# Kernel optimization log

Measured on AMD Instinct MI355X. Metric: run time of the kernel, lower is better.

The kernel has to match this reference:

```python
import jax, jax.numpy as jnp
import numpy as np

H, D = 8, 8          # num_heads, hidden_size (head dim)
SCALE = 0.25         # Hopfield beta/scaling
STEPS = 3            # update_steps_max
LN_EPS = 1e-5


def ln(x, g, b):
    m = x.mean(-1, keepdims=True)
    v = ((x - m) ** 2).mean(-1, keepdims=True)
    return (x - m) * jax.lax.rsqrt(v + LN_EPS) * g + b


def setup_inputs() -> dict:
    key = jax.random.key(0)
    ks = jax.random.split(key, 8)
    B, N, E = 32, 512, 512
    P = H * D  # 64 virtual hopfield dim
    s = lambda k, shape: jax.random.normal(k, shape, jnp.float32) * 0.05
    return dict(
        x=jax.random.normal(ks[0], (B, N, E), jnp.float32),
        g_q=jnp.ones((E,), jnp.float32), b_q=jnp.zeros((E,), jnp.float32),
        g_k=jnp.ones((E,), jnp.float32), b_k=jnp.zeros((E,), jnp.float32),
        g_v=jnp.ones((E,), jnp.float32), b_v=jnp.zeros((E,), jnp.float32),
        Wq=s(ks[1], (P, E)), bq=jnp.zeros((P,), jnp.float32),
        Wk=s(ks[2], (P, E)), bk=jnp.zeros((P,), jnp.float32),
        Wv=s(ks[3], (P, E)), bv=jnp.zeros((P,), jnp.float32),
        Wo=s(ks[4], (E, P)), bo=jnp.zeros((E,), jnp.float32),
        Wl=s(ks[5], (1, N * E)), bl=jnp.zeros((1,), jnp.float32),
    )


def reference(x, g_q, b_q, g_k, b_k, g_v, b_v,
              Wq, bq, Wk, bk, Wv, bv, Wo, bo, Wl, bl):
    B, N, E = x.shape
    # LayerNorm on state (query), stored (key), projection (value) patterns
    q = (ln(x, g_q, b_q) @ Wq.T + bq).reshape(B, N, H, D)
    k = (ln(x, g_k, b_k) @ Wk.T + bk).reshape(B, N, H, D)
    v = (ln(x, g_v, b_v) @ Wv.T + bv).reshape(B, N, H, D)
    # iterative Hopfield retrieval: xi <- softmax(beta * xi K^T) K
    xi = q
    for _ in range(STEPS):
        a = jax.nn.softmax(SCALE * jnp.einsum('bihd,bjhd->bhij', xi, k), axis=-1)
        xi = jnp.einsum('bhij,bjhd->bihd', a, k)
    # final association with value patterns
    a = jax.nn.softmax(SCALE * jnp.einsum('bihd,bjhd->bhij', xi, k), axis=-1)
    o = jnp.einsum('bhij,bjhd->bihd', a, v).reshape(B, N, H * D)
    o = o @ Wo.T + bo              # (B, N, E) out projection
    y = o.reshape(B, N * E) @ Wl.T + bl  # (B, 1) classifier head
    return y.reshape(-1)           # flatten(start_dim=0) -> (B,)
```

## Files before the change

### kernel.cpp

```cpp
#include <hip/hip_runtime.h>

#define E_DIM 512
#define N_DIM 512
#define B_DIM 32
#define H_DIM 8
#define D_DIM 8
#define P3    192

typedef _Float16 half_t;
typedef __attribute__((ext_vector_type(2))) _Float16 half2v;
typedef __attribute__((ext_vector_type(4))) _Float16 half4v;
typedef __attribute__((ext_vector_type(8))) _Float16 half8v;
typedef __attribute__((ext_vector_type(4))) float f32x4;

#define XS_STRIDE 520

#define SM_KT0 0
#define SM_KB0 4800
#define SM_Z0  8896
#define SM_XI0 9408
#define SM_TOT 9936
#define KT_STRIDE 532

__device__ inline float block_reduce_256(float v) {
    __shared__ float red[4];
    #pragma unroll
    for (int m = 32; m >= 1; m >>= 1) v += __shfl_xor(v, m);
    int w = threadIdx.x >> 6;
    if ((threadIdx.x & 63) == 0) red[w] = v;
    __syncthreads();
    if (threadIdx.x == 0) v = red[0] + red[1] + red[2] + red[3];
    return v;
}

__device__ inline half8v cvt8(float4 a, float4 b) {
    half8v h;
    h[0] = (half_t)a.x; h[1] = (half_t)a.y; h[2] = (half_t)a.z; h[3] = (half_t)a.w;
    h[4] = (half_t)b.x; h[5] = (half_t)b.y; h[6] = (half_t)b.z; h[7] = (half_t)b.w;
    return h;
}

__device__ inline half2v pk2(float a, float b) {
    return __builtin_bit_cast(half2v, __builtin_amdgcn_cvt_pkrtz(a, b));
}

__global__ __launch_bounds__(256) void prep_w(const float* __restrict__ Wq,
                        const float* __restrict__ Wk, const float* __restrict__ Wv,
                        const float* __restrict__ gq, const float* __restrict__ gk,
                        const float* __restrict__ gv,
                        const float* __restrict__ bnq, const float* __restrict__ bnk,
                        const float* __restrict__ bnv,
                        const float* __restrict__ bq, const float* __restrict__ bk,
                        const float* __restrict__ bv,
                        const float* __restrict__ bl,
                        half_t* __restrict__ WthF, float* __restrict__ colsum,
                        float* __restrict__ b2, float* __restrict__ y,
                        float* __restrict__ c0acc) {
    int pp = blockIdx.x;
    int which = pp >> 6, p = pp & 63;
    int ct = pp >> 4, c16 = pp & 15;
    const float* W  = (which == 0) ? Wq  : (which == 1) ? Wk  : Wv;
    const float* g  = (which == 0) ? gq  : (which == 1) ? gk  : gv;
    const float* bn = (which == 0) ? bnq : (which == 1) ? bnk : bnv;
    const float* bb = (which == 0) ? bq  : (which == 1) ? bk  : bv;
    int t = threadIdx.x;
    if (pp == 0) {
        if (t < 32) y[t] = bl[0];
        if (t == 32) c0acc[0] = 0.f;
    }
    float cs = 0.f, dt = 0.f;
    #pragma unroll
    for (int l = 0; l < 2; ++l) {
        int e = t + l * 256;
        float wv = W[p * E_DIM + e];
        half_t wh = (half_t)(wv * g[e]);
        int k32 = e >> 5, g2 = (e >> 3) & 3, j = e & 7;
        WthF[(((size_t)(ct * 16 + k32) * 64) + g2 * 16 + c16) * 8 + j] = wh;
        cs += (float)wh;
        dt += wv * bn[e];
    }
    cs = block_reduce_256(cs);
    __syncthreads();
    dt = block_reduce_256(dt);
    if (t == 0) { colsum[pp] = cs; b2[pp] = dt + bb[p]; }
}

__global__ __launch_bounds__(256) void ln_qkv_wl2(const float* __restrict__ x,
                                              const half_t* __restrict__ WthF,
                                              const float* __restrict__ b2,
                                              const float* __restrict__ colsum,
                                              half_t* __restrict__ qkv16,
                                              const float* __restrict__ Wl,
                                              const float* __restrict__ Wo,
                                              const float* __restrict__ bo,
                                              float* __restrict__ Wl2,
                                              float* __restrict__ c0acc) {
    __shared__ half_t Xs[16 * XS_STRIDE];
    __shared__ float stats[16][2];
    if (blockIdx.x < 1024) {
        const int t = threadIdx.x;
        const int lane = t & 63;
        const int w = t >> 6;
        const int g2 = lane >> 4, c16 = lane & 15;
        const int row0 = blockIdx.x * 16;
        {
            const int row = t >> 4, c = t & 15;
            const float4* xrow = (const float4*)(x + (size_t)(row0 + row) * E_DIM);
            float sx = 0.f, sxx = 0.f;
            #pragma unroll
            for (int l = 0; l < 8; ++l) {
                int f4 = c + l * 16;
                float4 a = xrow[f4];
                sx  += a.x + a.y + a.z + a.w;
                sxx += a.x*a.x + a.y*a.y + a.z*a.z + a.w*a.w;
                half4v h;
                h[0] = (half_t)a.x; h[1] = (half_t)a.y;
                h[2] = (half_t)a.z; h[3] = (half_t)a.w;
                *(half4v*)&Xs[row * XS_STRIDE + f4 * 4] = h;
            }
            #pragma unroll
            for (int m = 1; m <= 8; m <<= 1) {
                sx += __shfl_xor(sx, m); sxx += __shfl_xor(sxx, m);
            }
            if (c == 0) {
                float mean = sx * (1.f / E_DIM);
                float var  = sxx * (1.f / E_DIM) - mean * mean;
                stats[row][0] = mean;
                stats[row][1] = rsqrtf(var + 1e-5f);
            }
        }
        __syncthreads();
        f32x4 acc[3] = {{0.f,0.f,0.f,0.f},{0.f,0.f,0.f,0.f},{0.f,0.f,0.f,0.f}};
        const half_t* wf = WthF + (size_t)w * 3 * 16 * 512;
        #pragma unroll 4
        for (int k32 = 0; k32 < 16; ++k32) {
            half8v af = *(const half8v*)&Xs[c16 * XS_STRIDE + k32 * 32 + g2 * 8];
            #pragma unroll
            for (int nt = 0; nt < 3; ++nt) {
                half8v bf = *(const half8v*)(wf + ((size_t)(nt * 16 + k32)) * 512 + lane * 8);
                acc[nt] = __builtin_amdgcn_mfma_f32_16x16x32_f16(af, bf, acc[nt], 0, 0, 0);
            }
        }
        #pragma unroll
        for (int nt = 0; nt < 3; ++nt) {
            int pp = w * 48 + nt * 16 + c16;
            float cs = colsum[pp], bb = b2[pp];
            int which = pp >> 6, p = pp & 63;
            int h = p >> 3, d = p & 7;
            half_t* dst0 = qkv16 + (size_t)which * (B_DIM * H_DIM * N_DIM * D_DIM);
            #pragma unroll
            for (int r = 0; r < 4; ++r) {
                int rowi = g2 * 4 + r;
                float val = stats[rowi][1] * (acc[nt][r] - stats[rowi][0] * cs) + bb;
                int ng = row0 + rowi;
                int b = ng >> 9, n = ng & 511;
                dst0[(((size_t)(b * H_DIM + h)) * N_DIM + n) * D_DIM + d] = (half_t)val;
            }
        }
    } else {
        const int blk = blockIdx.x - 1024;
        const int t = threadIdx.x;
        const int lane = t & 63;
        const int w = t >> 6;
        const int g2 = lane >> 4, c16 = lane & 15;
        const int n0 = blk * 16;
        const int pcol = w * 16;
        f32x4 acc = {0.f, 0.f, 0.f, 0.f};
        float pc = 0.f;
        const float* arow = Wl + (size_t)(n0 + c16) * E_DIM;
        #pragma unroll 2
        for (int k0 = 0; k0 < E_DIM; k0 += 32) {
            int kbase = k0 + g2 * 8;
            float4 a0 = *(const float4*)(arow + kbase);
            float4 a1 = *(const float4*)(arow + kbase + 4);
            if (w == 0) {
                float4 b0 = *(const float4*)(bo + kbase);
                float4 b1 = *(const float4*)(bo + kbase + 4);
                pc += a0.x*b0.x + a0.y*b0.y + a0.z*b0.z + a0.w*b0.w
                    + a1.x*b1.x + a1.y*b1.y + a1.z*b1.z + a1.w*b1.w;
            }
            half8v af = cvt8(a0, a1);
            half8v bf;
            #pragma unroll
            for (int j = 0; j < 8; ++j)
                bf[j] = (half_t)Wo[(size_t)(kbase + j) * 64 + pcol + c16];
            acc = __builtin_amdgcn_mfma_f32_16x16x32_f16(af, bf, acc, 0, 0, 0);
        }
        int p = pcol + c16, h = p >> 3, d = p & 7;
        #pragma unroll
        for (int r = 0; r < 4; ++r) {
            int n = n0 + g2 * 4 + r;
            Wl2[h * (N_DIM * D_DIM) + n * D_DIM + d] = acc[r];
        }
        if (w == 0) {
            pc += __shfl_xor(pc, 16); pc += __shfl_xor(pc, 32);
            pc += __shfl_xor(pc, 1);  pc += __shfl_xor(pc, 2);
            pc += __shfl_xor(pc, 4);  pc += __shfl_xor(pc, 8);
            if (lane == 0) atomicAdd(c0acc, pc);
        }
    }
}

__global__ __launch_bounds__(256, 8) void hopfield(const half_t* __restrict__ q16,
                                                   const half_t* __restrict__ k16,
                                                   const half_t* __restrict__ v16,
                                                   const float* __restrict__ Wl2,
                                                   const float* __restrict__ c0acc,
                                                   float* __restrict__ y) {
    __shared__ __align__(16) half_t sm[SM_TOT];
    const int t = threadIdx.x;
    const int lane = t & 63;
    const int w = t >> 6;
    const int g2 = lane >> 4;
    const int c16 = lane & 15;
    const int bh = blockIdx.x >> 3, seg = blockIdx.x & 7;
    const float C = 0.25f * 1.44269504088896f;
    const half_t* kg = k16 + (size_t)bh * (N_DIM * D_DIM);
    const half_t* vg = v16 + (size_t)bh * (N_DIM * D_DIM);
    const half_t* qg = q16 + (size_t)bh * (N_DIM * D_DIM) + seg * 64 * 8;
    const float* wl2p = Wl2 + (bh & 7) * (N_DIM * D_DIM) + seg * 64 * 8;

    {
        const int j0 = 2 * t;
        half8v r0 = *(const half8v*)(kg + j0 * 8);
        half8v r1 = *(const half8v*)(kg + j0 * 8 + 8);
        *(half8v*)&sm[SM_KB0 + j0 * 8]     = r0;
        *(half8v*)&sm[SM_KB0 + j0 * 8 + 8] = r1;
        #pragma unroll
        for (int d = 0; d < 8; ++d) {
            half2v p; p[0] = r0[d]; p[1] = r1[d];
            *(half2v*)&sm[SM_KT0 + d * KT_STRIDE + j0] = p;
        }
        half2v one2; one2[0] = (half_t)1.f; one2[1] = (half_t)1.f;
        *(half2v*)&sm[SM_KT0 + 8 * KT_STRIDE + j0] = one2;
        if (t < 128) {
            const half4v z4 = {};
            *(half4v*)&sm[SM_Z0 + t * 4] = z4;
        }
        if (t < 6) {
            half2v z2 = {};
            *(half2v*)&sm[9 * KT_STRIDE + t * 2] = z2;
        }
        if (t < 64) {
            half8v hq = *(const half8v*)(qg + t * 8);
            half8v h;
            #pragma unroll
            for (int d = 0; d < 8; ++d) h[d] = (half_t)(C * (float)hq[d]);
            *(half8v*)&sm[SM_XI0 + t * 8] = h;
        }
    }
    __syncthreads();

    const half_t* aTp  = sm + SM_KT0 + c16 * KT_STRIDE + g2 * 4;
    const half_t* akp0 = sm + ((g2 < 2) ? (SM_KB0 + c16 * 8 + g2 * 4) : SM_Z0);
    const int akstep4  = (g2 < 2) ? 512 : 0;
    const f32x4 Zf = {0.f, 0.f, 0.f, 0.f};
    const half4v hz = {};
    float fsum = 0.f;

    for (int it = 0; it < 4; ++it) {
        if (it == 3) {
            __syncthreads();
            const int j0 = 2 * t;
            half8v r0 = *(const half8v*)(vg + j0 * 8);
            half8v r1 = *(const half8v*)(vg + j0 * 8 + 8);
            #pragma unroll
            for (int d = 0; d < 8; ++d) {
                half2v p; p[0] = r0[d]; p[1] = r1[d];
                *(half2v*)&sm[SM_KT0 + d * KT_STRIDE + j0] = p;
            }
            __syncthreads();
        }
        half4v bx = *(const half4v*)&sm[SM_XI0 + (w * 16 + c16) * 8 + g2 * 4];
        if (g2 >= 2) bx = hz;
        f32x4 U = Zf;
        const half_t* ap = akp0;
        #pragma unroll 2
        for (int k4 = 0; k4 < 8; ++k4) {
            #pragma unroll
            for (int u = 0; u < 4; ++u) {
                const int kt = k4 * 4 + u;
                half4v ak = *(const half4v*)(ap + u * 128);
                half4v aT = *(const half4v*)(aTp + kt * 16);
                f32x4 S = __builtin_amdgcn_mfma_f32_16x16x16f16(ak, bx, Zf, 0, 0, 0);
                half2v lo = pk2(__builtin_amdgcn_exp2f(S[0]), __builtin_amdgcn_exp2f(S[1]));
                half2v hi = pk2(__builtin_amdgcn_exp2f(S[2]), __builtin_amdgcn_exp2f(S[3]));
                half4v p = __builtin_shufflevector(lo, hi, 0, 1, 2, 3);
                U = __builtin_amdgcn_mfma_f32_16x16x16f16(aT, p, U, 0, 0, 0);
            }
            ap += akstep4;
        }
        float den = __shfl(U[0], 32 + c16, 64);
        float inv = __builtin_amdgcn_rcpf(den);
        if (it < 3) {
            if (g2 < 2) {
                half4v h;
                #pragma unroll
                for (int r = 0; r < 4; ++r) h[r] = (half_t)(U[r] * (C * inv));
                *(half4v*)&sm[SM_XI0 + (w * 16 + c16) * 8 + g2 * 4] = h;
            }
        } else {
            if (g2 < 2) {
                float4 w0 = *(const float4*)&wl2p[(w * 16 + c16) * 8 + g2 * 4];
                fsum = inv * (U[0]*w0.x + U[1]*w0.y + U[2]*w0.z + U[3]*w0.w);
            }
        }
    }
    float tot = block_reduce_256(fsum);
    if (t == 0) atomicAdd(&y[bh >> 3], tot);
    if (blockIdx.x == 0 && t < 32) {
        atomicAdd(&y[t], c0acc[0]);
    }
}

extern "C" void kernel_launch(void* const* d_in, const int* in_sizes, int n_in,
                              void* d_out, int out_size, void* d_ws, size_t ws_size,
                              hipStream_t stream) {
    const float* x   = (const float*)d_in[0];
    const float* g_q = (const float*)d_in[1];
    const float* b_q = (const float*)d_in[2];
    const float* g_k = (const float*)d_in[3];
    const float* b_k = (const float*)d_in[4];
    const float* g_v = (const float*)d_in[5];
    const float* b_v = (const float*)d_in[6];
    const float* Wq  = (const float*)d_in[7];
    const float* bq  = (const float*)d_in[8];
    const float* Wk  = (const float*)d_in[9];
    const float* bk  = (const float*)d_in[10];
    const float* Wv  = (const float*)d_in[11];
    const float* bv  = (const float*)d_in[12];
    const float* Wo  = (const float*)d_in[13];
    const float* bo  = (const float*)d_in[14];
    const float* Wl  = (const float*)d_in[15];
    const float* bl  = (const float*)d_in[16];
    float* out = (float*)d_out;

    float* ws = (float*)d_ws;
    float*  colsum = ws;
    float*  b2     = ws + 192;
    float*  c0acc  = ws + 384;
    float*  Wl2    = ws + 448;
    half_t* WthF   = (half_t*)(ws + 33216);
    half_t* qkv16  = (half_t*)(ws + 82368);

    half_t* q16 = qkv16;
    half_t* k16 = qkv16 + 1048576;
    half_t* v16 = qkv16 + 2097152;

    prep_w    <<<192, 256, 0, stream>>>(Wq, Wk, Wv, g_q, g_k, g_v,
                                        b_q, b_k, b_v, bq, bk, bv, bl,
                                        WthF, colsum, b2, out, c0acc);
    ln_qkv_wl2<<<1056, 256, 0, stream>>>(x, WthF, b2, colsum, qkv16,
                                         Wl, Wo, bo, Wl2, c0acc);
    hopfield  <<<2048, 256, 0, stream>>>(q16, k16, v16, Wl2, c0acc, out);
}
```

Before: 159.7 us.

## Rewrite Hopfield attention with 32x32x16 MFMA and register-resident queries

Moves the Hopfield retrieval loop from 16x16x16 MFMA tiles to 32x32x16 tiles. Each block now handles 128 query rows, so the grid halves to 1024 blocks. The softmax weights and the updated xi stay in registers, passed between lanes with permlane32 swaps instead of a shared-memory round trip. K and V are both staged into shared memory up front in one tiled transposed layout, which removes the mid-loop V reload and its extra barriers. The query scaling moves into the QKV projection epilogue. The aim is better MFMA utilisation and less LDS and barrier traffic, at the cost of more registers, a lower occupancy target (launch bounds 4) and a larger LDS footprint.

```diff
diff --git a/kernel.cpp b/kernel.cpp
--- a/kernel.cpp
+++ b/kernel.cpp
@@ -12,15 +12,17 @@
 typedef __attribute__((ext_vector_type(4))) _Float16 half4v;
 typedef __attribute__((ext_vector_type(8))) _Float16 half8v;
 typedef __attribute__((ext_vector_type(4))) float f32x4;
+typedef __attribute__((ext_vector_type(16))) float f32x16;
+typedef __attribute__((ext_vector_type(2))) unsigned int u32x2;
+typedef __attribute__((ext_vector_type(4))) unsigned int u32x4;
 
 #define XS_STRIDE 520
+#define CQ 0.3606737602222409f
 
 #define SM_KT0 0
-#define SM_KB0 4800
-#define SM_Z0  8896
-#define SM_XI0 9408
-#define SM_TOT 9936
-#define KT_STRIDE 532
+#define SM_VT0 4608
+#define SM_KB0 9216
+#define SM_TOT 13312
 
 __device__ inline float block_reduce_256(float v) {
     __shared__ float red[4];
@@ -40,8 +42,19 @@
     return h;
 }
 
-__device__ inline half2v pk2(float a, float b) {
-    return __builtin_bit_cast(half2v, __builtin_amdgcn_cvt_pkrtz(a, b));
+__device__ inline unsigned pku(float a, float b) {
+    return __builtin_bit_cast(unsigned, __builtin_amdgcn_cvt_pkrtz(a, b));
+}
+
+__device__ inline void plswap(unsigned &a, unsigned &b) {
+    u32x2 r = __builtin_amdgcn_permlane32_swap(a, b, false, false);
+    a = r[0]; b = r[1];
+}
+
+__device__ inline float bcast_lo(float v) {
+    unsigned u = __builtin_bit_cast(unsigned, v);
+    u32x2 r = __builtin_amdgcn_permlane32_swap(u, u, false, false);
+    return __builtin_bit_cast(float, r[0]);
 }
 
 __global__ __launch_bounds__(256) void prep_w(const float* __restrict__ Wq,
@@ -145,13 +158,14 @@
         for (int nt = 0; nt < 3; ++nt) {
             int pp = w * 48 + nt * 16 + c16;
             float cs = colsum[pp], bb = b2[pp];
+            float qsc = (w * 3 + nt < 4) ? CQ : 1.0f;
             int which = pp >> 6, p = pp & 63;
             int h = p >> 3, d = p & 7;
             half_t* dst0 = qkv16 + (size_t)which * (B_DIM * H_DIM * N_DIM * D_DIM);
             #pragma unroll
             for (int r = 0; r < 4; ++r) {
                 int rowi = g2 * 4 + r;
-                float val = stats[rowi][1] * (acc[nt][r] - stats[rowi][0] * cs) + bb;
+                float val = (stats[rowi][1] * (acc[nt][r] - stats[rowi][0] * cs) + bb) * qsc;
                 int ng = row0 + rowi;
                 int b = ng >> 9, n = ng & 511;
                 dst0[(((size_t)(b * H_DIM + h)) * N_DIM + n) * D_DIM + d] = (half_t)val;
@@ -201,7 +215,7 @@
     }
 }
 
-__global__ __launch_bounds__(256, 8) void hopfield(const half_t* __restrict__ q16,
+__global__ __launch_bounds__(256, 4) void hopfield(const half_t* __restrict__ q16,
                                                    const half_t* __restrict__ k16,
                                                    const half_t* __restrict__ v16,
                                                    const float* __restrict__ Wl2,
@@ -211,99 +225,91 @@
     const int t = threadIdx.x;
     const int lane = t & 63;
     const int w = t >> 6;
-    const int g2 = lane >> 4;
-    const int c16 = lane & 15;
-    const int bh = blockIdx.x >> 3, seg = blockIdx.x & 7;
-    const float C = 0.25f * 1.44269504088896f;
+    const int lq = lane & 31;
+    const int hi = lane >> 5;
+    const int bh = blockIdx.x >> 2, seg = blockIdx.x & 3;
     const half_t* kg = k16 + (size_t)bh * (N_DIM * D_DIM);
     const half_t* vg = v16 + (size_t)bh * (N_DIM * D_DIM);
-    const half_t* qg = q16 + (size_t)bh * (N_DIM * D_DIM) + seg * 64 * 8;
-    const float* wl2p = Wl2 + (bh & 7) * (N_DIM * D_DIM) + seg * 64 * 8;
+    const half_t* qg = q16 + (size_t)bh * (N_DIM * D_DIM) + seg * 128 * 8;
+    const float* wl2p = Wl2 + (bh & 7) * (N_DIM * D_DIM) + seg * 128 * 8;
 
     {
         const int j0 = 2 * t;
         half8v r0 = *(const half8v*)(kg + j0 * 8);
         half8v r1 = *(const half8v*)(kg + j0 * 8 + 8);
+        half8v v0 = *(const half8v*)(vg + j0 * 8);
+        half8v v1 = *(const half8v*)(vg + j0 * 8 + 8);
         *(half8v*)&sm[SM_KB0 + j0 * 8]     = r0;
         *(half8v*)&sm[SM_KB0 + j0 * 8 + 8] = r1;
+        const int kt = t >> 2, jp = j0 & 7;
+        half_t* kb = &sm[SM_KT0 + kt * 72 + jp];
+        half_t* vb = &sm[SM_VT0 + kt * 72 + jp];
         #pragma unroll
         for (int d = 0; d < 8; ++d) {
-            half2v p; p[0] = r0[d]; p[1] = r1[d];
-            *(half2v*)&sm[SM_KT0 + d * KT_STRIDE + j0] = p;
+            half2v pk_; pk_[0] = r0[d]; pk_[1] = r1[d];
+            *(half2v*)(kb + d * 8) = pk_;
+            half2v pv_; pv_[0] = v0[d]; pv_[1] = v1[d];
+            *(half2v*)(vb + d * 8) = pv_;
         }
         half2v one2; one2[0] = (half_t)1.f; one2[1] = (half_t)1.f;
-        *(half2v*)&sm[SM_KT0 + 8 * KT_STRIDE + j0] = one2;
-        if (t < 128) {
-            const half4v z4 = {};
-            *(half4v*)&sm[SM_Z0 + t * 4] = z4;
-        }
-        if (t < 6) {
-            half2v z2 = {};
-            *(half2v*)&sm[9 * KT_STRIDE + t * 2] = z2;
-        }
-        if (t < 64) {
-            half8v hq = *(const half8v*)(qg + t * 8);
-            half8v h;
-            #pragma unroll
-            for (int d = 0; d < 8; ++d) h[d] = (half_t)(C * (float)hq[d]);
-            *(half8v*)&sm[SM_XI0 + t * 8] = h;
-        }
+        *(half2v*)(kb + 64) = one2;
+        *(half2v*)(vb + 64) = one2;
     }
     __syncthreads();
 
-    const half_t* aTp  = sm + SM_KT0 + c16 * KT_STRIDE + g2 * 4;
-    const half_t* akp0 = sm + ((g2 < 2) ? (SM_KB0 + c16 * 8 + g2 * 4) : SM_Z0);
-    const int akstep4  = (g2 < 2) ? 512 : 0;
-    const f32x4 Zf = {0.f, 0.f, 0.f, 0.f};
-    const half4v hz = {};
+    const half_t* akbase = sm + SM_KB0 + (hi ? 0 : lq * 8);
+    const int akstep = hi ? 0 : 256;
+    int rowc = lq & 15; if (rowc > 8) rowc = 8;
+    const half_t* aTk = sm + SM_KT0 + hi * 72 + rowc * 8;
+    const f32x16 Zf16 = {};
     float fsum = 0.f;
 
+    half8v bx;
+    {
+        half8v bq = *(const half8v*)(qg + (w * 32 + lq) * 8);
+        u32x4 qw = __builtin_bit_cast(u32x4, bq);
+        if (hi) { qw[0] = 0u; qw[1] = 0u; qw[2] = 0u; qw[3] = 0u; }
+        bx = __builtin_bit_cast(half8v, qw);
+    }
+
     for (int it = 0; it < 4; ++it) {
-        if (it == 3) {
-            __syncthreads();
-            const int j0 = 2 * t;
-            half8v r0 = *(const half8v*)(vg + j0 * 8);
-            half8v r1 = *(const half8v*)(vg + j0 * 8 + 8);
-            #pragma unroll
-            for (int d = 0; d < 8; ++d) {
-                half2v p; p[0] = r0[d]; p[1] = r1[d];
-                *(half2v*)&sm[SM_KT0 + d * KT_STRIDE + j0] = p;
-            }
-            __syncthreads();
-        }
-        half4v bx = *(const half4v*)&sm[SM_XI0 + (w * 16 + c16) * 8 + g2 * 4];
-        if (g2 >= 2) bx = hz;
-        f32x4 U = Zf;
-        const half_t* ap = akp0;
-        #pragma unroll 2
-        for (int k4 = 0; k4 < 8; ++k4) {
-            #pragma unroll
-            for (int u = 0; u < 4; ++u) {
-                const int kt = k4 * 4 + u;
-                half4v ak = *(const half4v*)(ap + u * 128);
-                half4v aT = *(const half4v*)(aTp + kt * 16);
-                f32x4 S = __builtin_amdgcn_mfma_f32_16x16x16f16(ak, bx, Zf, 0, 0, 0);
-                half2v lo = pk2(__builtin_amdgcn_exp2f(S[0]), __builtin_amdgcn_exp2f(S[1]));
-                half2v hi = pk2(__builtin_amdgcn_exp2f(S[2]), __builtin_amdgcn_exp2f(S[3]));
-                half4v p = __builtin_shufflevector(lo, hi, 0, 1, 2, 3);
-                U = __builtin_amdgcn_mfma_f32_16x16x16f16(aT, p, U, 0, 0, 0);
-            }
-            ap += akstep4;
-        }
-        float den = __shfl(U[0], 32 + c16, 64);
-        float inv = __builtin_amdgcn_rcpf(den);
+        const half_t* aTit = aTk + (it == 3 ? (SM_VT0 - SM_KT0) : 0);
+        const half_t* akp = akbase;
+        f32x16 U = {};
+        for (int tile = 0; tile < 16; ++tile) {
+            half8v ak = *(const half8v*)akp;
+            akp += akstep;
+            half8v aT0 = *(const half8v*)(aTit + tile * 288);
+            half8v aT1 = *(const half8v*)(aTit + tile * 288 + 144);
+            f32x16 S = __builtin_amdgcn_mfma_f32_32x32x16_f16(ak, bx, Zf16, 0, 0, 0);
+            unsigned wa = pku(__builtin_amdgcn_exp2f(S[0]),  __builtin_amdgcn_exp2f(S[1]));
+            unsigned wb = pku(__builtin_amdgcn_exp2f(S[2]),  __builtin_amdgcn_exp2f(S[3]));
+            unsigned wc = pku(__builtin_amdgcn_exp2f(S[4]),  __builtin_amdgcn_exp2f(S[5]));
+            unsigned wd = pku(__builtin_amdgcn_exp2f(S[6]),  __builtin_amdgcn_exp2f(S[7]));
+            unsigned we = pku(__builtin_amdgcn_exp2f(S[8]),  __builtin_amdgcn_exp2f(S[9]));
+            unsigned wf = pku(__builtin_amdgcn_exp2f(S[10]), __builtin_amdgcn_exp2f(S[11]));
+            unsigned wg = pku(__builtin_amdgcn_exp2f(S[12]), __builtin_amdgcn_exp2f(S[13]));
+            unsigned wh = pku(__builtin_amdgcn_exp2f(S[14]), __builtin_amdgcn_exp2f(S[15]));
+            plswap(wa, wc); plswap(wb, wd);
+            plswap(we, wg); plswap(wf, wh);
+            u32x4 c0 = {wa, wb, wc, wd};
+            u32x4 c1 = {we, wf, wg, wh};
+            U = __builtin_amdgcn_mfma_f32_32x32x16_f16(aT0, __builtin_bit_cast(half8v, c0), U, 0, 0, 0);
+            U = __builtin_amdgcn_mfma_f32_32x32x16_f16(aT1, __builtin_bit_cast(half8v, c1), U, 0, 0, 0);
+        }
+        float inv = __builtin_amdgcn_rcpf(bcast_lo(U[4]));
         if (it < 3) {
-            if (g2 < 2) {
-                half4v h;
-                #pragma unroll
-                for (int r = 0; r < 4; ++r) h[r] = (half_t)(U[r] * (C * inv));
-                *(half4v*)&sm[SM_XI0 + (w * 16 + c16) * 8 + g2 * 4] = h;
-            }
+            float ci = CQ * inv;
+            unsigned W01 = pku(U[0] * ci, U[1] * ci);
+            unsigned W23 = pku(U[2] * ci, U[3] * ci);
+            unsigned z1 = 0u, z2 = 0u;
+            plswap(W01, z1);
+            plswap(W23, z2);
+            u32x4 nb = {W01, W23, z1, z2};
+            bx = __builtin_bit_cast(half8v, nb);
         } else {
-            if (g2 < 2) {
-                float4 w0 = *(const float4*)&wl2p[(w * 16 + c16) * 8 + g2 * 4];
-                fsum = inv * (U[0]*w0.x + U[1]*w0.y + U[2]*w0.z + U[3]*w0.w);
-            }
+            float4 wv = *(const float4*)&wl2p[(w * 32 + lq) * 8 + hi * 4];
+            fsum = inv * (U[0] * wv.x + U[1] * wv.y + U[2] * wv.z + U[3] * wv.w);
         }
     }
     float tot = block_reduce_256(fsum);
@@ -352,5 +358,5 @@
                                         WthF, colsum, b2, out, c0acc);
     ln_qkv_wl2<<<1056, 256, 0, stream>>>(x, WthF, b2, colsum, qkv16,
                                          Wl, Wo, bo, Wl2, c0acc);
-    hopfield  <<<2048, 256, 0, stream>>>(q16, k16, v16, Wl2, c0acc, out);
-}
+    hopfield  <<<1024, 256, 0, stream>>>(q16, k16, v16, Wl2, c0acc, out);
+}
```

Result: faster. 155.9 us (-2.4%).
